# Optimization experiments

Measured on AMD Instinct MI355X. Metric: run time of the kernel, lower is better.

## Reference

```python
import jax, jax.numpy as jnp
import numpy as np

N_FFT = 1024
HOP = 256
WIN = N_FFT  # win_length = n_fft in VocosISTFTHead
PAD = (WIN - HOP) // 2  # 384, 'same' padding trim
CLAMP_MAX = 100.0


def _hann_periodic(n):
    # matches torch.hann_window(n, periodic=True)
    return 0.5 * (1.0 - jnp.cos(2.0 * jnp.pi * jnp.arange(n, dtype=jnp.float32) / n))


def setup_inputs() -> dict:
    key = jax.random.key(0)
    k1, k2, k3 = jax.random.split(key, 3)
    B, T, H = 16, 2048, 512
    hidden_states = jax.random.normal(k1, (B, T, H), dtype=jnp.float32)
    # out_proj: Linear(hidden_dim, n_fft+2); scaled so exp(magnitude) stays sane
    W = jax.random.normal(k2, (N_FFT + 2, H), dtype=jnp.float32) * 0.02
    b = jax.random.normal(k3, (N_FFT + 2,), dtype=jnp.float32) * 0.02
    window = _hann_periodic(WIN)
    return {"hidden_states": hidden_states, "W": W, "b": b, "window": window}


def reference(hidden_states, W, b, window):
    B, T, _ = hidden_states.shape
    # linear projection -> [B, T, n_fft+2] -> transpose -> [B, n_fft+2, T]
    spec = (hidden_states @ W.T + b).transpose(0, 2, 1)
    half = (N_FFT + 2) // 2  # n_fft//2 + 1 = 513 freq bins
    magnitude = jnp.minimum(jnp.exp(spec[:, :half]), CLAMP_MAX)
    phase = spec[:, half:]
    coeffs = magnitude * (jnp.cos(phase) + 1j * jnp.sin(phase))  # [B, F, T] complex
    # inverse rfft along freq axis, norm='backward' (default) -> [B, n_fft, T]
    frames = jnp.fft.irfft(coeffs, n=N_FFT, axis=1)
    frames = frames * window[None, :, None]
    L = (T - 1) * HOP + WIN
    idx = (jnp.arange(T)[:, None] * HOP + jnp.arange(WIN)[None, :]).reshape(-1)
    frames_flat = frames.transpose(0, 2, 1).reshape(B, -1)
    audio = jnp.zeros((B, L), frames.dtype).at[:, idx].add(frames_flat)
    # NOLA normalization: overlap-added squared window
    wsq = jnp.broadcast_to(window ** 2, (T, WIN)).reshape(-1)
    norm = jnp.zeros((L,), window.dtype).at[idx].add(wsq)
    return audio[:, PAD:-PAD] / norm[PAD:-PAD]
```

## Files before the change

kernel.cpp:

```cpp
#include <hip/hip_runtime.h>
#include <hip/hip_fp16.h>
#include <math.h>
#include <stdint.h>


#define FRAMES  32768
#define TWO_PI  6.283185307179586f
#define FPB 12
#define SPB 9
#define BPB 228

typedef unsigned short ushort_t;
typedef __attribute__((ext_vector_type(8))) _Float16 f16x8;
typedef __attribute__((ext_vector_type(4))) float f32x4;

#define GLDS(gp, lp) __builtin_amdgcn_global_load_lds( \
    (const __attribute__((address_space(1))) void*)(gp), \
    (__attribute__((address_space(3))) void*)(lp), 16, 0, 0)

__device__ __forceinline__ float2 f2(float x, float y){ return make_float2(x,y); }
__device__ __forceinline__ float2 cadd(float2 a, float2 b){ return f2(a.x+b.x, a.y+b.y); }
__device__ __forceinline__ float2 csub(float2 a, float2 b){ return f2(a.x-b.x, a.y-b.y); }
__device__ __forceinline__ float2 cmul(float2 a, float2 b){ return f2(a.x*b.x - a.y*b.y, a.x*b.y + a.y*b.x); }

__device__ __forceinline__ uint32_t pack2h(float a, float b) {
  const ushort_t ha = __half_as_ushort(__float2half_rn(a));
  const ushort_t hb = __half_as_ushort(__float2half_rn(b));
  return (uint32_t)ha | ((uint32_t)hb << 16);
}

__global__ __launch_bounds__(256) void convert_AB(
    const float* __restrict__ hs, const float* __restrict__ Wm,
    const float* __restrict__ bias, ushort_t* __restrict__ Af,
    ushort_t* __restrict__ Whi, __half* __restrict__ coeffs)
{
  const int bid = blockIdx.x;
  const int t = threadIdx.x;
  if (bid < 2048) {
    const int r = t >> 4, c = t & 15;
    const int m = bid * 16 + r;
    const float* src = hs + (size_t)m * 512 + c * 32;
    const float* wm  = Wm + (size_t)512  * 512 + c * 32;
    const float* wp  = Wm + (size_t)1025 * 512 + c * 32;

    float v[32];
    #pragma unroll
    for (int i = 0; i < 8; ++i) *(float4*)&v[i*4] = *(const float4*)(src + i*4);

    float dm = 0.f, dp = 0.f;
    #pragma unroll
    for (int i = 0; i < 8; ++i) {
      const float4 a  = *(const float4*)&v[i*4];
      const float4 m4 = *(const float4*)(wm + i*4);
      const float4 p4 = *(const float4*)(wp + i*4);
      dm = fmaf(a.x,m4.x, fmaf(a.y,m4.y, fmaf(a.z,m4.z, fmaf(a.w,m4.w, dm))));
      dp = fmaf(a.x,p4.x, fmaf(a.y,p4.y, fmaf(a.z,p4.z, fmaf(a.w,p4.w, dp))));
    }

    uint32_t hu[16];
    #pragma unroll
    for (int i = 0; i < 16; ++i) hu[i] = pack2h(v[2*i], v[2*i+1]);
    ushort_t* dh = Af + (size_t)m * 512 + c * 32;
    #pragma unroll
    for (int q = 0; q < 4; ++q)
      *(uint4*)(dh + q*8) = make_uint4(hu[4*q], hu[4*q+1], hu[4*q+2], hu[4*q+3]);

    #pragma unroll
    for (int off = 8; off; off >>= 1) {
      dm += __shfl_xor(dm, off, 16);
      dp += __shfl_xor(dp, off, 16);
    }
    if (c == 0) {
      const float sm = dm + bias[512], sp = dp + bias[1025];
      const float mag = fminf(__expf(sm), 100.0f);
      coeffs[(size_t)m * 1024 + 1] = __float2half_rn(mag * __cosf(sp));
    }
  } else {
    const int gid = (bid - 2048) * 256 + t;
    const int sd = gid & 3;
    const int r  = (gid >> 2) & 255;
    const int kt = (gid >> 10) & 15;
    const int yb = gid >> 14;
    const int srow = (r < 128) ? (yb*128 + r) : (513 + yb*128 + (r - 128));
    const float* src = Wm + (size_t)srow * 512 + kt*32 + sd*8;
    const float4 a = *(const float4*)src;
    const float4 b = *(const float4*)(src + 4);
    const uint4 o = make_uint4(pack2h(a.x,a.y), pack2h(a.z,a.w),
                               pack2h(b.x,b.y), pack2h(b.z,b.w));
    *(uint4*)(Whi + (size_t)gid * 8) = o;
  }
}

__global__ __launch_bounds__(512, 2) void gemm_mfma(
    const ushort_t* __restrict__ Af, const ushort_t* __restrict__ Whi,
    const float* __restrict__ bias, __half* __restrict__ coeffs)
{
  __shared__ ushort_t Ab[24576];

  const int tid = threadIdx.x;
  const int w = tid >> 6, l = tid & 63;
  const int wr = w >> 2, wc = w & 3;
  const int lc = l & 15, kg = l >> 4;

  const int bid = blockIdx.x;
  const int swz = (bid & 7) * 64 + (bid >> 3);
  const int mb = swz >> 2, yb = swz & 3;

  uint32_t pa_off[2], lofs[2];
  #pragma unroll
  for (int ch = 0; ch < 2; ++ch) {
    const int g = ch*512 + tid;
    const int r = g >> 2, sd = g & 3;
    lofs[ch] = r*32 + sd*8;
    const int sl = sd ^ ((r >> 1) & 3);
    pa_off[ch] = (uint32_t)(mb*256 + r)*512 + sl*8;
  }
  uint32_t pb_off[4];
  #pragma unroll
  for (int cf = 0; cf < 4; ++cf) {
    const int rB = ((cf < 2) ? 0 : 128) + wc*32 + (cf & 1)*16 + lc;
    pb_off[cf] = (uint32_t)yb*131072u + rB*32 + kg*8;
  }

  f32x4 acc[8][4];
  #pragma unroll
  for (int rf = 0; rf < 8; ++rf)
    #pragma unroll
    for (int cf = 0; cf < 4; ++cf)
      #pragma unroll
      for (int q = 0; q < 4; ++q) acc[rf][cf][q] = 0.f;

  const int asl = (kg ^ ((lc >> 1) & 3)) * 8;

  f16x8 p[4], q[4];

#define WAITV2 asm volatile("s_waitcnt vmcnt(2) lgkmcnt(0)" ::: "memory")
#define WAITV0 asm volatile("s_waitcnt vmcnt(0) lgkmcnt(0)" ::: "memory")
#define SB     __builtin_amdgcn_s_barrier()
#define SCH0   __builtin_amdgcn_sched_barrier(0)

#define DSREAD(DST, BASE, RF0) do {                                      \
    _Pragma("unroll")                                                    \
    for (int r4 = 0; r4 < 4; ++r4) {                                     \
      const int rr = wr*128 + ((RF0) + r4)*16 + lc;                      \
      DST[r4] = *(const f16x8*)(&Ab[(BASE) + rr*32 + asl]);              \
    }                                                                    \
  } while (0)

#define MFMA16(FA, RF0, RB) do {                                         \
    __builtin_amdgcn_s_setprio(1);                                       \
    _Pragma("unroll")                                                    \
    for (int r4 = 0; r4 < 4; ++r4)                                       \
      _Pragma("unroll")                                                  \
      for (int cf = 0; cf < 4; ++cf)                                     \
        acc[(RF0)+r4][cf] = __builtin_amdgcn_mfma_f32_16x16x32_f16(      \
            FA[r4], RB[cf], acc[(RF0)+r4][cf], 0, 0, 0);                 \
    __builtin_amdgcn_s_setprio(0);                                       \
  } while (0)

#define ITER(KT, RBC, RBN, LAST) do {                                    \
    if (LAST) { WAITV0; } else { WAITV2; }                               \
    SB;                                                                  \
    DSREAD(q, aR, 4);                                                    \
    if ((KT) < 14) GLDS(Af + pa_off[0] + ((KT)+2)*32, &Ab[aW + lofs[0]]);\
    if ((KT) < 15) {                                                     \
      RBN[0] = *(const f16x8*)(Whi + pb_off[0] + ((KT)+1)*8192);         \
      RBN[1] = *(const f16x8*)(Whi + pb_off[1] + ((KT)+1)*8192);         \
    }                                                                    \
    SCH0;                                                                \
    MFMA16(p, 0, RBC);                                                   \
    if ((KT) < 15) DSREAD(p, aN, 0);                                     \
    if ((KT) < 14) GLDS(Af + pa_off[1] + ((KT)+2)*32, &Ab[aW + lofs[1]]);\
    if ((KT) < 15) {                                                     \
      RBN[2] = *(const f16x8*)(Whi + pb_off[2] + ((KT)+1)*8192);         \
      RBN[3] = *(const f16x8*)(Whi + pb_off[3] + ((KT)+1)*8192);         \
    }                                                                    \
    SCH0;                                                                \
    MFMA16(q, 4, RBC);                                                   \
    { const unsigned t_ = aR; aR = aN; aN = aW; aW = t_; }               \
  } while (0)

  f16x8 rb0[4], rb1[4];
  GLDS(Af + pa_off[0], &Ab[lofs[0]]);
  GLDS(Af + pa_off[1], &Ab[lofs[1]]);
  GLDS(Af + pa_off[0] + 32, &Ab[8192 + lofs[0]]);
  GLDS(Af + pa_off[1] + 32, &Ab[8192 + lofs[1]]);
  SCH0;
  #pragma unroll
  for (int j = 0; j < 4; ++j) rb0[j] = *(const f16x8*)(Whi + pb_off[j]);
  SCH0;
  asm volatile("s_waitcnt vmcnt(6)" ::: "memory");
  SB;
  unsigned aR = 0, aN = 8192, aW = 16384;
  DSREAD(p, aR, 0);

  for (int k2 = 0; k2 < 8; ++k2) {
    ITER(2*k2,     rb0, rb1, false);
    ITER(2*k2 + 1, rb1, rb0, k2 == 7);
  }
#undef ITER
#undef DSREAD
#undef MFMA16

  const int pc0 = yb*128 + wc*32 + lc;
  const int pc1 = pc0 + 16;
  const float bm0 = bias[pc0], bp0 = bias[513 + pc0];
  const float bm1 = bias[pc1], bp1 = bias[513 + pc1];
  #pragma unroll
  for (int rf = 0; rf < 8; ++rf) {
    const int rbase = mb*256 + wr*128 + rf*16 + kg*4;
    #pragma unroll
    for (int qi = 0; qi < 4; ++qi) {
      __half* row = coeffs + (size_t)(rbase + qi) * 1024;
      {
        const float sm = acc[rf][0][qi] + bm0;
        const float sp = acc[rf][2][qi] + bp0;
        const float mag = fminf(__expf(sm), 100.0f);
        const float aa = mag * __cosf(sp);
        const float bb = mag * __sinf(sp);
        if (pc0 == 0) row[0] = __float2half_rn(aa);
        else *(__half2*)(row + 2*pc0) = __float22half2_rn(make_float2(aa, bb));
      }
      {
        const float sm = acc[rf][1][qi] + bm1;
        const float sp = acc[rf][3][qi] + bp1;
        const float mag = fminf(__expf(sm), 100.0f);
        const float aa = mag * __cosf(sp);
        const float bb = mag * __sinf(sp);
        *(__half2*)(row + 2*pc1) = __float22half2_rn(make_float2(aa, bb));
      }
    }
  }
}

#define PIDX(s) ((s) + ((s) >> 3))
#define WFENCE  __builtin_amdgcn_wave_barrier()

template<int NS>
__device__ __forceinline__ void stage_fft(const float2* in, float2* out, int l)
{
  float2 v[8];
  #pragma unroll
  for (int r = 0; r < 8; ++r) v[r] = in[PIDX(l + 64*r)];
  if (NS > 1) {
    const float ang = TWO_PI * (float)(l & (NS-1)) / (float)(NS * 8);
    float sn, cs; __sincosf(ang, &sn, &cs);
    const float2 wb = f2(cs, sn);
    float2 cur = wb;
    #pragma unroll
    for (int r = 1; r < 8; ++r) { v[r] = cmul(v[r], cur); cur = cmul(cur, wb); }
  }
  const float2 e0=v[0], e1=v[2], e2=v[4], e3=v[6];
  const float2 o0=v[1], o1=v[3], o2=v[5], o3=v[7];
  float2 a = cadd(e0,e2), b = csub(e0,e2), c = cadd(e1,e3), d = csub(e1,e3);
  const float2 E0 = cadd(a,c), E2 = csub(a,c);
  const float2 E1 = f2(b.x - d.y, b.y + d.x), E3 = f2(b.x + d.y, b.y - d.x);
  a = cadd(o0,o2); b = csub(o0,o2); c = cadd(o1,o3); d = csub(o1,o3);
  const float2 O0 = cadd(a,c), O2 = csub(a,c);
  const float2 O1 = f2(b.x - d.y, b.y + d.x), O3 = f2(b.x + d.y, b.y - d.x);
  const float r2 = 0.70710678118654752f;
  const float2 t0 = O0;
  const float2 t1 = f2(r2*(O1.x - O1.y),  r2*(O1.x + O1.y));
  const float2 t2 = f2(-O2.y, O2.x);
  const float2 t3 = f2(-r2*(O3.x + O3.y), r2*(O3.x - O3.y));
  float2 X[8];
  X[0]=cadd(E0,t0); X[4]=csub(E0,t0);
  X[1]=cadd(E1,t1); X[5]=csub(E1,t1);
  X[2]=cadd(E2,t2); X[6]=csub(E2,t2);
  X[3]=cadd(E3,t3); X[7]=csub(E3,t3);
  const int idxD = (l / NS) * (NS * 8) + (l & (NS-1));
  #pragma unroll
  for (int q = 0; q < 8; ++q) out[PIDX(idxD + q*NS)] = X[q];
}

__device__ __forceinline__ void stage_last(const float2* in, __half* frout,
                                           const float* __restrict__ window, int l)
{
  float2 v[8];
  #pragma unroll
  for (int r = 0; r < 8; ++r) v[r] = in[PIDX(l + 64*r)];
  {
    const float ang = TWO_PI * (float)l / 512.0f;
    float sn, cs; __sincosf(ang, &sn, &cs);
    const float2 wb = f2(cs, sn);
    float2 cur = wb;
    #pragma unroll
    for (int r = 1; r < 8; ++r) { v[r] = cmul(v[r], cur); cur = cmul(cur, wb); }
  }
  const float2 e0=v[0], e1=v[2], e2=v[4], e3=v[6];
  const float2 o0=v[1], o1=v[3], o2=v[5], o3=v[7];
  float2 a = cadd(e0,e2), b = csub(e0,e2), c = cadd(e1,e3), d = csub(e1,e3);
  const float2 E0 = cadd(a,c), E2 = csub(a,c);
  const float2 E1 = f2(b.x - d.y, b.y + d.x), E3 = f2(b.x + d.y, b.y - d.x);
  a = cadd(o0,o2); b = csub(o0,o2); c = cadd(o1,o3); d = csub(o1,o3);
  const float2 O0 = cadd(a,c), O2 = csub(a,c);
  const float2 O1 = f2(b.x - d.y, b.y + d.x), O3 = f2(b.x + d.y, b.y - d.x);
  const float r2 = 0.70710678118654752f;
  const float2 t0 = O0;
  const float2 t1 = f2(r2*(O1.x - O1.y),  r2*(O1.x + O1.y));
  const float2 t2 = f2(-O2.y, O2.x);
  const float2 t3 = f2(-r2*(O3.x + O3.y), r2*(O3.x - O3.y));
  float2 X[8];
  X[0]=cadd(E0,t0); X[4]=csub(E0,t0);
  X[1]=cadd(E1,t1); X[5]=csub(E1,t1);
  X[2]=cadd(E2,t2); X[6]=csub(E2,t2);
  X[3]=cadd(E3,t3); X[7]=csub(E3,t3);
  #pragma unroll
  for (int q = 0; q < 8; ++q) {
    const int m = l + 64*q;
    const float2 wv = *(const float2*)(window + 2*m);
    *(__half2*)&frout[2*m] =
        __float22half2_rn(make_float2(X[q].x * wv.x, X[q].y * wv.y));
  }
}

__global__ __launch_bounds__(256) void fft_oa(
    const __half* __restrict__ coeffs, const float* __restrict__ window,
    float* __restrict__ out)
{
  __shared__ float2 bA[4][576];
  __shared__ float2 bB[4][576];
  __shared__ __half fr[FPB][1024];

  const int tid = threadIdx.x;
  const int w = tid >> 6, l = tid & 63;
  const int bid = blockIdx.x;
  const int b = bid / BPB, j = bid - b * BPB;
  const int f0 = SPB * j - 3;
  const float sc = 1.0f / 1024.0f;

  for (int i = 0; i < 3; ++i) {
    const int lf = 3*w + i;
    const int f  = f0 + lf;
    if (f < 0 || f > 2047) {
      #pragma unroll
      for (int jj = 0; jj < 8; ++jj)
        *(__half2*)&fr[lf][2*(l + 64*jj)] = __half2();
      continue;
    }
    const __half2* crow = (const __half2*)(coeffs + (size_t)(b*2048 + f) * 1024);
    #pragma unroll
    for (int jj = 0; jj < 4; ++jj) {
      const int k = 1 + l + 64*jj;
      const float2 Ck = __half22float2(crow[k]);
      const float2 Cq = __half22float2(crow[512-k]);
      float sn, cs; __sincosf(TWO_PI * (1.0f/1024.0f) * (float)k, &sn, &cs);
      const float Ex = sc*(Ck.x + Cq.x), Ey = sc*(Ck.y - Cq.y);
      const float Dx = Ck.x - Cq.x,      Dy = Ck.y + Cq.y;
      const float Ox = sc*(cs*Dx - sn*Dy), Oy = sc*(cs*Dy + sn*Dx);
      bA[w][PIDX(k)]     = f2(Ex - Oy, Ey + Ox);
      bA[w][PIDX(512-k)] = f2(Ex + Oy, Ox - Ey);
    }
    if (l == 0) {
      const float2 dn = __half22float2(crow[0]);
      bA[w][PIDX(0)] = f2(sc*(dn.x + dn.y), sc*(dn.x - dn.y));
    }
    WFENCE;
    stage_fft<1>(bA[w], bB[w], l);
    WFENCE;
    stage_fft<8>(bB[w], bA[w], l);
    WFENCE;
    stage_last(bA[w], fr[lf], window, l);
    WFENCE;
  }
  __syncthreads();

  float wsq[4];
  #pragma unroll
  for (int i = 0; i < 4; ++i) {
    const float wv = window[tid + 256*i];
    wsq[i] = wv * wv;
  }
  float* outb = out + (size_t)b * 524288;
  #pragma unroll
  for (int k = 0; k < SPB; ++k) {
    const int t = SPB*j + k;
    const int o = 256*t + tid - 384;
    float acc = 0.f, nrm = 0.f;
    #pragma unroll
    for (int i = 0; i < 4; ++i) {
      const int f = t - i;
      if (f >= 0 && f <= 2047) {
        acc += __half2float(fr[k + 3 - i][tid + 256*i]);
        nrm += wsq[i];
      }
    }
    if (o >= 0 && o < 524288) outb[o] = acc / nrm;
  }
}

extern "C" void kernel_launch(void* const* d_in, const int* in_sizes, int n_in,
                              void* d_out, int out_size, void* d_ws, size_t ws_size,
                              hipStream_t stream)
{
  const float* hs     = (const float*)d_in[0];
  const float* Wm     = (const float*)d_in[1];
  const float* bias   = (const float*)d_in[2];
  const float* window = (const float*)d_in[3];

  char* base = (char*)d_ws;
  ushort_t* Af     = (ushort_t*)base;
  ushort_t* Whi    = (ushort_t*)(base + 33554432);
  __half*   coeffs = (__half*)(base + 67108864);

  convert_AB<<<2304, 256, 0, stream>>>(hs, Wm, bias, Af, Whi, coeffs);
  gemm_mfma<<<512,  512, 0, stream>>>(Af, Whi, bias, coeffs);
  fft_oa<<<16 * BPB, 256, 0, stream>>>(coeffs, window, (float*)d_out);
}
```

Before: 145.3 us.

## Stream frames through ring buffer to cut redundant halo FFTs in overlap-add

The FFT/overlap-add kernel now gives each block a long run of 44 output segments, processed in rounds of 4. Each round computes 4 new frames into an 8-slot shared ring buffer, and the 3 halo frames are computed only once per block. Before, each block recomputed 3 halo frames for every 9 outputs, so this removes most of the redundant inverse FFT work. In exchange the grid shrinks to 752 blocks, which may reduce occupancy and load balance, and each round adds two block-wide barriers.

```diff
diff --git a/kernel.cpp b/kernel.cpp
--- a/kernel.cpp
+++ b/kernel.cpp
@@ -6,9 +6,9 @@
 
 #define FRAMES  32768
 #define TWO_PI  6.283185307179586f
-#define FPB 12
-#define SPB 9
-#define BPB 228
+#define SPR 4
+#define RND 11
+#define JB  47
 
 typedef unsigned short ushort_t;
 typedef __attribute__((ext_vector_type(8))) _Float16 f16x8;
@@ -314,56 +314,55 @@
   }
 }
 
+__device__ __forceinline__ void fft_frame(const __half* __restrict__ cb, int F,
+                                          float2* bAw, float2* bBw,
+                                          __half (*fr)[1024],
+                                          const float* __restrict__ window, int l)
+{
+  if (F < 0 || F > 2047) return;
+  const __half2* crow = (const __half2*)(cb + (size_t)F * 1024);
+  const float sc = 1.0f / 1024.0f;
+  #pragma unroll
+  for (int jj = 0; jj < 4; ++jj) {
+    const int k = 1 + l + 64*jj;
+    const float2 Ck = __half22float2(crow[k]);
+    const float2 Cq = __half22float2(crow[512-k]);
+    float sn, cs; __sincosf(TWO_PI * (1.0f/1024.0f) * (float)k, &sn, &cs);
+    const float Ex = sc*(Ck.x + Cq.x), Ey = sc*(Ck.y - Cq.y);
+    const float Dx = Ck.x - Cq.x,      Dy = Ck.y + Cq.y;
+    const float Ox = sc*(cs*Dx - sn*Dy), Oy = sc*(cs*Dy + sn*Dx);
+    bAw[PIDX(k)]     = f2(Ex - Oy, Ey + Ox);
+    bAw[PIDX(512-k)] = f2(Ex + Oy, Ox - Ey);
+  }
+  if (l == 0) {
+    const float2 dn = __half22float2(crow[0]);
+    bAw[PIDX(0)] = f2(sc*(dn.x + dn.y), sc*(dn.x - dn.y));
+  }
+  WFENCE;
+  stage_fft<1>(bAw, bBw, l);
+  WFENCE;
+  stage_fft<8>(bBw, bAw, l);
+  WFENCE;
+  stage_last(bAw, fr[F & 7], window, l);
+  WFENCE;
+}
+
 __global__ __launch_bounds__(256) void fft_oa(
     const __half* __restrict__ coeffs, const float* __restrict__ window,
     float* __restrict__ out)
 {
   __shared__ float2 bA[4][576];
   __shared__ float2 bB[4][576];
-  __shared__ __half fr[FPB][1024];
+  __shared__ __half fr[8][1024];
 
   const int tid = threadIdx.x;
   const int w = tid >> 6, l = tid & 63;
   const int bid = blockIdx.x;
-  const int b = bid / BPB, j = bid - b * BPB;
-  const int f0 = SPB * j - 3;
-  const float sc = 1.0f / 1024.0f;
-
-  for (int i = 0; i < 3; ++i) {
-    const int lf = 3*w + i;
-    const int f  = f0 + lf;
-    if (f < 0 || f > 2047) {
-      #pragma unroll
-      for (int jj = 0; jj < 8; ++jj)
-        *(__half2*)&fr[lf][2*(l + 64*jj)] = __half2();
-      continue;
-    }
-    const __half2* crow = (const __half2*)(coeffs + (size_t)(b*2048 + f) * 1024);
-    #pragma unroll
-    for (int jj = 0; jj < 4; ++jj) {
-      const int k = 1 + l + 64*jj;
-      const float2 Ck = __half22float2(crow[k]);
-      const float2 Cq = __half22float2(crow[512-k]);
-      float sn, cs; __sincosf(TWO_PI * (1.0f/1024.0f) * (float)k, &sn, &cs);
-      const float Ex = sc*(Ck.x + Cq.x), Ey = sc*(Ck.y - Cq.y);
-      const float Dx = Ck.x - Cq.x,      Dy = Ck.y + Cq.y;
-      const float Ox = sc*(cs*Dx - sn*Dy), Oy = sc*(cs*Dy + sn*Dx);
-      bA[w][PIDX(k)]     = f2(Ex - Oy, Ey + Ox);
-      bA[w][PIDX(512-k)] = f2(Ex + Oy, Ox - Ey);
-    }
-    if (l == 0) {
-      const float2 dn = __half22float2(crow[0]);
-      bA[w][PIDX(0)] = f2(sc*(dn.x + dn.y), sc*(dn.x - dn.y));
-    }
-    WFENCE;
-    stage_fft<1>(bA[w], bB[w], l);
-    WFENCE;
-    stage_fft<8>(bB[w], bA[w], l);
-    WFENCE;
-    stage_last(bA[w], fr[lf], window, l);
-    WFENCE;
-  }
-  __syncthreads();
+  const int b = bid / JB, j = bid - b * JB;
+  const int T0 = SPR * RND * j;
+
+  const __half* cb = coeffs + (size_t)b * 2048 * 1024;
+  float* outb = out + (size_t)b * 524288;
 
   float wsq[4];
   #pragma unroll
@@ -371,21 +370,28 @@
     const float wv = window[tid + 256*i];
     wsq[i] = wv * wv;
   }
-  float* outb = out + (size_t)b * 524288;
-  #pragma unroll
-  for (int k = 0; k < SPB; ++k) {
-    const int t = SPB*j + k;
-    const int o = 256*t + tid - 384;
-    float acc = 0.f, nrm = 0.f;
-    #pragma unroll
-    for (int i = 0; i < 4; ++i) {
-      const int f = t - i;
-      if (f >= 0 && f <= 2047) {
-        acc += __half2float(fr[k + 3 - i][tid + 256*i]);
-        nrm += wsq[i];
+
+  if (w < 3) fft_frame(cb, T0 - 3 + w, bA[w], bB[w], fr, window, l);
+
+  for (int r = 0; r < RND; ++r) {
+    fft_frame(cb, T0 + SPR*r + w, bA[w], bB[w], fr, window, l);
+    __syncthreads();
+    #pragma unroll
+    for (int k = 0; k < SPR; ++k) {
+      const int s = T0 + SPR*r + k;
+      const int o = 256*s + tid - 384;
+      float acc = 0.f, nrm = 0.f;
+      #pragma unroll
+      for (int i = 0; i < 4; ++i) {
+        const int f = s - i;
+        if (f >= 0 && f <= 2047) {
+          acc += __half2float(fr[f & 7][tid + 256*i]);
+          nrm += wsq[i];
+        }
       }
+      if (o >= 0 && o < 524288) outb[o] = acc / nrm;
     }
-    if (o >= 0 && o < 524288) outb[o] = acc / nrm;
+    __syncthreads();
   }
 }
 
@@ -405,5 +411,5 @@
 
   convert_AB<<<2304, 256, 0, stream>>>(hs, Wm, bias, Af, Whi, coeffs);
   gemm_mfma<<<512,  512, 0, stream>>>(Af, Whi, bias, coeffs);
-  fft_oa<<<16 * BPB, 256, 0, stream>>>(coeffs, window, (float*)d_out);
-}
+  fft_oa<<<16 * JB, 256, 0, stream>>>(coeffs, window, (float*)d_out);
+}
```

Result: faster. 133.2 us (-8.3%).
